# Optimization experiments

Measured on AMD Instinct MI355X. Metric: run time of the kernel, lower is better.

Reference implementation:

```python
import jax, jax.numpy as jnp
import numpy as np
from jax import lax

GAMMA = 1.0
B = 10            # forced by qnn_arch[0]=10 via w1 @ x in feedforward
N_TRAIN = 8192    # kernel support set size


def setup_inputs() -> dict:
    key = jax.random.key(0)
    ks = jax.random.split(key, 20)
    x = jax.random.normal(ks[0], (B, 3, 250, 250), jnp.float32)
    # CNN params (He-ish scale)
    conv1_w = jax.random.normal(ks[1], (6, 3, 5, 5), jnp.float32) * 0.1
    conv1_b = jax.random.normal(ks[2], (6,), jnp.float32) * 0.01
    conv2_w = jax.random.normal(ks[3], (15, 6, 3, 3), jnp.float32) * 0.1
    conv2_b = jax.random.normal(ks[4], (15,), jnp.float32) * 0.01
    fc1_w = jax.random.normal(ks[5], (120, 55815), jnp.float32) * 0.004
    fc1_b = jax.random.normal(ks[6], (120,), jnp.float32) * 0.01
    fc2_w = jax.random.normal(ks[7], (84, 120), jnp.float32) * 0.09
    fc2_b = jax.random.normal(ks[8], (84,), jnp.float32) * 0.01
    fc3_w = jax.random.normal(ks[9], (1, 84), jnp.float32) * 0.1
    fc3_b = jax.random.normal(ks[10], (1,), jnp.float32) * 0.01
    # QNN weights (original uses plain randn)
    qnn_w1 = jax.random.normal(ks[11], (20, 10), jnp.float32)
    qnn_w2 = jax.random.normal(ks[12], (5, 20), jnp.float32)
    # Precomputed training states: tanh(w2 @ tanh(w1 @ f)) per random feature f
    feats = jax.random.normal(ks[13], (N_TRAIN, 10), jnp.float32)
    train_states = jnp.tanh(jnp.tanh(feats @ qnn_w1.T) @ qnn_w2.T)  # [N_TRAIN, 5]
    kcls_w = jax.random.normal(ks[14], (2, N_TRAIN), jnp.float32) * 0.01
    kcls_b = jax.random.normal(ks[15], (2,), jnp.float32) * 0.01
    return {
        'x': x,
        'conv1_w': conv1_w, 'conv1_b': conv1_b,
        'conv2_w': conv2_w, 'conv2_b': conv2_b,
        'fc1_w': fc1_w, 'fc1_b': fc1_b,
        'fc2_w': fc2_w, 'fc2_b': fc2_b,
        'fc3_w': fc3_w, 'fc3_b': fc3_b,
        'qnn_w1': qnn_w1, 'qnn_w2': qnn_w2,
        'train_states': train_states,
        'kcls_w': kcls_w, 'kcls_b': kcls_b,
    }


def _conv(h, w, b, stride, pad):
    out = lax.conv_general_dilated(
        h, w, (stride, stride), [(pad, pad), (pad, pad)],
        dimension_numbers=('NCHW', 'OIHW', 'NCHW'))
    return out + b[None, :, None, None]


def _maxpool_2s1(h):
    return lax.reduce_window(h, -jnp.inf, lax.max, (1, 1, 2, 2), (1, 1, 1, 1), 'VALID')


def reference(x, conv1_w, conv1_b, conv2_w, conv2_b, fc1_w, fc1_b,
              fc2_w, fc2_b, fc3_w, fc3_b, qnn_w1, qnn_w2,
              train_states, kcls_w, kcls_b):
    h = jax.nn.relu(_conv(x, conv1_w, conv1_b, 2, 1))   # [10,6,124,124]
    h = _maxpool_2s1(h)                                 # [10,6,123,123]
    h = jax.nn.relu(_conv(h, conv2_w, conv2_b, 2, 1))   # [10,15,62,62]
    h = _maxpool_2s1(h)                                 # [10,15,61,61]
    h = h.reshape(h.shape[0], -1)                       # [10,55815]
    h = jax.nn.relu(h @ fc1_w.T + fc1_b)                # [10,120]
    h = jax.nn.relu(h @ fc2_w.T + fc2_b)                # [10,84]
    h = h @ fc3_w.T + fc3_b                             # [10,1]
    # QNN feedforward: batch dim B=10 is consumed as the qnn input dim
    s = jnp.tanh(qnn_w1 @ h)                            # [20,1]
    s = jnp.tanh(qnn_w2 @ s)                            # [5,1]
    fs = s[:, 0]                                        # [5]
    # Batched RBF kernel against all train states (replaces the Python .item() loop)
    d2 = jnp.sum((fs[None, :] - train_states) ** 2, axis=-1)  # [N_TRAIN]
    K = jnp.exp(-GAMMA * d2)                            # [N_TRAIN]
    out = K[None, :] @ kcls_w.T + kcls_b                # [1,2]
    return out
```

## Files before the change

### kernel.cpp

```cpp
#include <hip/hip_runtime.h>


#define ACT_STRIDE 55816

__global__ __launch_bounds__(256) void convpool1_k(
    const float* __restrict__ x, const float* __restrict__ w,
    const float* __restrict__ bias, float* __restrict__ out ) {
    const int b   = blockIdx.x;
    const int py0 = blockIdx.y * 4;
    const int px0 = blockIdx.z * 64;
    const int iy0 = 2 * py0 - 1;
    const int ix0 = 2 * px0 - 1;

    __shared__ float sx[3][13][136];

    const int tid = threadIdx.x;

    for (int j = tid; j < 3 * 13 * 133; j += 256) {
        int c  = j % 133;
        int r  = (j / 133) % 13;
        int ic = j / (133 * 13);
        int ix = ix0 + c, iy = iy0 + r;
        float v = 0.f;
        if ((unsigned)ix < 250u && (unsigned)iy < 250u)
            v = x[((size_t)(b * 3 + ic) * 250 + iy) * 250 + ix];
        sx[ic][r][c] = v;
    }
    __syncthreads();

    const int pxl = tid & 63;
    const int pyl = tid >> 6;
    const int py = py0 + pyl, px = px0 + pxl;

    float acc[6][4];
    #pragma unroll
    for (int o = 0; o < 6; ++o) {
        float bv = bias[o];
        #pragma unroll
        for (int q = 0; q < 4; ++q) acc[o][q] = bv;
    }

    #pragma unroll
    for (int ic = 0; ic < 3; ++ic) {
        #pragma unroll
        for (int r = 0; r < 7; ++r) {
            #pragma unroll
            for (int c = 0; c < 7; ++c) {
                float xv = sx[ic][2 * pyl + r][2 * pxl + c];
                #pragma unroll
                for (int dy = 0; dy < 2; ++dy) {
                    int ky = r - 2 * dy;
                    if (ky < 0 || ky >= 5) continue;
                    #pragma unroll
                    for (int dx = 0; dx < 2; ++dx) {
                        int kx = c - 2 * dx;
                        if (kx < 0 || kx >= 5) continue;
                        #pragma unroll
                        for (int o = 0; o < 6; ++o)
                            acc[o][dy * 2 + dx] =
                                fmaf(w[((o * 3 + ic) * 5 + ky) * 5 + kx], xv,
                                     acc[o][dy * 2 + dx]);
                    }
                }
            }
        }
    }

    if (py < 123 && px < 123) {
        #pragma unroll
        for (int o = 0; o < 6; ++o) {
            float m = fmaxf(fmaxf(acc[o][0], acc[o][1]),
                            fmaxf(acc[o][2], acc[o][3]));
            out[((size_t)(b * 6 + o) * 123 + py) * 123 + px] = fmaxf(m, 0.f);
        }
    }
}

__global__ __launch_bounds__(128) void convpool2_k(
    const float* __restrict__ in , const float* __restrict__ w,
    const float* __restrict__ bias, float* __restrict__ out ) {
    const int b   = blockIdx.x;
    const int py0 = blockIdx.y * 2;
    const int px0 = blockIdx.z * 31;
    const int n_py = (61 - py0) < 2 ? (61 - py0) : 2;
    const int n_oy = n_py + 1;
    const int iy0 = 2 * py0 - 1;
    const int ix0 = 2 * px0 - 1;

    __shared__ float sx[6][7][68];
    __shared__ float so[15][3][32];

    const int tid = threadIdx.x;

    for (int j = tid; j < 6 * 7 * 65; j += 128) {
        int col = j % 65;
        int r   = (j / 65) % 7;
        int ic  = j / (65 * 7);
        int ix = ix0 + col, iy = iy0 + r;
        float v = 0.f;
        if ((unsigned)ix < 123u && (unsigned)iy < 123u)
            v = in[((size_t)(b * 6 + ic) * 123 + iy) * 123 + ix];
        sx[ic][r][col] = v;
    }
    __syncthreads();

    for (int p = tid; p < n_oy * 32; p += 128) {
        int oxl = p & 31;
        int oyl = p >> 5;
        if (px0 + oxl < 62) {
            float acc[15];
            #pragma unroll
            for (int o = 0; o < 15; ++o) acc[o] = bias[o];
            #pragma unroll
            for (int ic = 0; ic < 6; ++ic) {
                #pragma unroll
                for (int ky = 0; ky < 3; ++ky) {
                    const float* xr = &sx[ic][2 * oyl + ky][2 * oxl];
                    #pragma unroll
                    for (int kx = 0; kx < 3; ++kx) {
                        float xv = xr[kx];
                        #pragma unroll
                        for (int o = 0; o < 15; ++o)
                            acc[o] += w[((o * 6 + ic) * 3 + ky) * 3 + kx] * xv;
                    }
                }
            }
            #pragma unroll
            for (int o = 0; o < 15; ++o) so[o][oyl][oxl] = fmaxf(acc[o], 0.f);
        }
    }
    __syncthreads();

    for (int j = tid; j < 15 * 2 * 31; j += 128) {
        int pxl = j % 31;
        int pyl = (j / 31) & 1;
        int oc  = j / 62;
        int px = px0 + pxl, py = py0 + pyl;
        if (pyl < n_py && px < 61) {
            float v = fmaxf(fmaxf(so[oc][pyl][pxl],     so[oc][pyl][pxl + 1]),
                            fmaxf(so[oc][pyl + 1][pxl], so[oc][pyl + 1][pxl + 1]));
            out[(size_t)b * ACT_STRIDE + ((size_t)oc * 61 + py) * 61 + px] = v;
        }
    }
}

#define FC1_K      55815
#define FC1_CHUNK  768
#define FC1_NC     73
#define FC1_RT     15

__global__ __launch_bounds__(256) void fc1_partial_k(
    const float* __restrict__ act ,
    const float* __restrict__ w   ,
    float* __restrict__ partials  ) {
    int rt  = blockIdx.x;
    int c   = blockIdx.y;
    int tid = threadIdx.x;
    int wave = tid >> 6, lane = tid & 63;
    int k0 = c * FC1_CHUNK;
    int k1 = k0 + FC1_CHUNK; if (k1 > FC1_K) k1 = FC1_K;
    int r0 = rt * 8 + wave * 2;
    const float* w0 = w + (size_t)r0 * FC1_K;
    const float* w1 = w + (size_t)(r0 + 1) * FC1_K;

    float acc0[10], acc1[10];
    #pragma unroll
    for (int b = 0; b < 10; ++b) { acc0[b] = 0.f; acc1[b] = 0.f; }

    for (int k = k0 + lane * 4; k < k1; k += 256) {
        if (k + 4 <= k1) {
            float4 a4[10];
            #pragma unroll
            for (int b = 0; b < 10; ++b)
                a4[b] = *reinterpret_cast<const float4*>(act + (size_t)b * ACT_STRIDE + k);
            float w00 = w0[k], w01 = w0[k + 1], w02 = w0[k + 2], w03 = w0[k + 3];
            float w10 = w1[k], w11 = w1[k + 1], w12 = w1[k + 2], w13 = w1[k + 3];
            #pragma unroll
            for (int b = 0; b < 10; ++b) {
                acc0[b] += w00 * a4[b].x + w01 * a4[b].y + w02 * a4[b].z + w03 * a4[b].w;
                acc1[b] += w10 * a4[b].x + w11 * a4[b].y + w12 * a4[b].z + w13 * a4[b].w;
            }
        } else {
            for (int j = 0; j < k1 - k; ++j) {
                float wv0 = w0[k + j], wv1 = w1[k + j];
                #pragma unroll
                for (int b = 0; b < 10; ++b) {
                    float av = act[(size_t)b * ACT_STRIDE + k + j];
                    acc0[b] += wv0 * av;
                    acc1[b] += wv1 * av;
                }
            }
        }
    }
    #pragma unroll
    for (int b = 0; b < 10; ++b) {
        float v0 = acc0[b], v1 = acc1[b];
        for (int off = 32; off > 0; off >>= 1) {
            v0 += __shfl_down(v0, off);
            v1 += __shfl_down(v1, off);
        }
        if (lane == 0) {
            size_t base = ((size_t)c * 120 + r0) * 10;
            partials[base + b]      = v0;
            partials[base + 10 + b] = v1;
        }
    }
}

__global__ __launch_bounds__(128) void fcA_k(
    const float* __restrict__ part , const float* __restrict__ fc1_b,
    const float* __restrict__ fc2_w, const float* __restrict__ fc2_b,
    const float* __restrict__ fc3_w, const float* __restrict__ fc3_b,
    float* __restrict__ h3 ) {
    const int b = blockIdx.x;
    const int tid = threadIdx.x;
    __shared__ float s_act[120];
    __shared__ float s_fc2[84];

    if (tid < 120) {
        float s = 0.f;
        for (int c = 0; c < FC1_NC; ++c) s += part[((size_t)c * 120 + tid) * 10 + b];
        s_act[tid] = fmaxf(s + fc1_b[tid], 0.f);
    }
    __syncthreads();
    if (tid < 84) {
        float acc = fc2_b[tid];
        #pragma unroll 4
        for (int k = 0; k < 120; ++k) acc += s_act[k] * fc2_w[tid * 120 + k];
        s_fc2[tid] = fmaxf(acc, 0.f);
    }
    __syncthreads();
    if (tid < 64) {
        float v = s_fc2[tid] * fc3_w[tid];
        if (tid < 20) v += s_fc2[tid + 64] * fc3_w[tid + 64];
        for (int off = 32; off > 0; off >>= 1) v += __shfl_down(v, off);
        if (tid == 0) h3[b] = v + fc3_b[0];
    }
}

__global__ __launch_bounds__(128) void clsB_k(
    const float* __restrict__ h3 ,
    const float* __restrict__ qw1, const float* __restrict__ qw2,
    const float* __restrict__ ts , const float* __restrict__ kw ,
    float* __restrict__ partials ) {
    int tid = threadIdx.x;
    __shared__ float s_h3[10], s_s1[20], s_fs[5];
    if (tid < 10) s_h3[tid] = h3[tid];
    __syncthreads();
    if (tid < 20) {
        float acc = 0.f;
        for (int b = 0; b < 10; ++b) acc += qw1[tid * 10 + b] * s_h3[b];
        s_s1[tid] = tanhf(acc);
    }
    __syncthreads();
    if (tid < 5) {
        float acc = 0.f;
        for (int j = 0; j < 20; ++j) acc += qw2[tid * 20 + j] * s_s1[j];
        s_fs[tid] = tanhf(acc);
    }
    __syncthreads();

    float f0 = s_fs[0], f1 = s_fs[1], f2 = s_fs[2], f3 = s_fs[3], f4 = s_fs[4];
    int n = blockIdx.x * 128 + tid;
    const float* t = ts + (size_t)n * 5;
    float d0 = f0 - t[0], d1 = f1 - t[1], d2 = f2 - t[2], d3 = f3 - t[3], d4 = f4 - t[4];
    float Kv = expf(-(d0 * d0 + d1 * d1 + d2 * d2 + d3 * d3 + d4 * d4));
    float a0 = Kv * kw[n];
    float a1 = Kv * kw[8192 + n];
    for (int off = 32; off > 0; off >>= 1) {
        a0 += __shfl_down(a0, off);
        a1 += __shfl_down(a1, off);
    }
    __shared__ float l0[2], l1[2];
    int wave = tid >> 6, lane = tid & 63;
    if (lane == 0) { l0[wave] = a0; l1[wave] = a1; }
    __syncthreads();
    if (tid == 0) {
        partials[blockIdx.x * 2 + 0] = l0[0] + l0[1];
        partials[blockIdx.x * 2 + 1] = l1[0] + l1[1];
    }
}

__global__ void clsC_k(const float* __restrict__ partials,
                       const float* __restrict__ kb, float* __restrict__ out) {
    int c = threadIdx.x;
    if (c < 2) {
        float acc = kb[c];
        for (int i = 0; i < 64; ++i) acc += partials[i * 2 + c];
        out[c] = acc;
    }
}

extern "C" void kernel_launch(void* const* d_in, const int* in_sizes, int n_in,
                              void* d_out, int out_size, void* d_ws, size_t ws_size,
                              hipStream_t stream) {
    const float* x        = (const float*)d_in[0];
    const float* conv1_w  = (const float*)d_in[1];
    const float* conv1_b  = (const float*)d_in[2];
    const float* conv2_w  = (const float*)d_in[3];
    const float* conv2_b  = (const float*)d_in[4];
    const float* fc1_w    = (const float*)d_in[5];
    const float* fc1_b    = (const float*)d_in[6];
    const float* fc2_w    = (const float*)d_in[7];
    const float* fc2_b    = (const float*)d_in[8];
    const float* fc3_w    = (const float*)d_in[9];
    const float* fc3_b    = (const float*)d_in[10];
    const float* qnn_w1   = (const float*)d_in[11];
    const float* qnn_w2   = (const float*)d_in[12];
    const float* tstates  = (const float*)d_in[13];
    const float* kcls_w   = (const float*)d_in[14];
    const float* kcls_b   = (const float*)d_in[15];

    float* ws = (float*)d_ws;
    float* p1       = ws;
    float* p2       = p1 + 907740;
    float* fc1_part = p2 + 558160;
    float* h3       = fc1_part + 87600;
    float* partials = h3 + 16;

    convpool1_k<<<dim3(10, 31, 2), 256, 0, stream>>>(x, conv1_w, conv1_b, p1);
    convpool2_k<<<dim3(10, 31, 2), 128, 0, stream>>>(p1, conv2_w, conv2_b, p2);
    fc1_partial_k<<<dim3(FC1_RT, FC1_NC), 256, 0, stream>>>(p2, fc1_w, fc1_part);
    fcA_k<<<10, 128, 0, stream>>>(fc1_part, fc1_b, fc2_w, fc2_b, fc3_w, fc3_b, h3);
    clsB_k<<<64, 128, 0, stream>>>(h3, qnn_w1, qnn_w2, tstates, kcls_w, partials);
    clsC_k<<<1, 64, 0, stream>>>(partials, kcls_b, (float*)d_out);
}
```

Measured before the change: 91.52 us.

## Restructure conv1 so each thread computes a conv-output column and pools via shuffles

```diff
diff --git a/kernel.cpp b/kernel.cpp
--- a/kernel.cpp
+++ b/kernel.cpp
@@ -7,19 +7,19 @@
     const float* __restrict__ x, const float* __restrict__ w,
     const float* __restrict__ bias, float* __restrict__ out ) {
     const int b   = blockIdx.x;
-    const int py0 = blockIdx.y * 4;
-    const int px0 = blockIdx.z * 64;
+    const int py0 = blockIdx.y * 8;
+    const int px0 = blockIdx.z * 63;
     const int iy0 = 2 * py0 - 1;
     const int ix0 = 2 * px0 - 1;
 
-    __shared__ float sx[3][13][136];
+    __shared__ float sx[3][21][132];
 
     const int tid = threadIdx.x;
 
-    for (int j = tid; j < 3 * 13 * 133; j += 256) {
-        int c  = j % 133;
-        int r  = (j / 133) % 13;
-        int ic = j / (133 * 13);
+    for (int j = tid; j < 3 * 21 * 131; j += 256) {
+        int c  = j % 131;
+        int r  = (j / 131) % 21;
+        int ic = j / (131 * 21);
         int ix = ix0 + c, iy = iy0 + r;
         float v = 0.f;
         if ((unsigned)ix < 250u && (unsigned)iy < 250u)
@@ -28,50 +28,50 @@
     }
     __syncthreads();
 
-    const int pxl = tid & 63;
-    const int pyl = tid >> 6;
-    const int py = py0 + pyl, px = px0 + pxl;
-
-    float acc[6][4];
-    #pragma unroll
-    for (int o = 0; o < 6; ++o) {
-        float bv = bias[o];
+    const int lane = tid & 63;
+    const int wv   = tid >> 6;
+
+    float acc[3][6];
+    #pragma unroll
+    for (int j = 0; j < 3; ++j)
         #pragma unroll
-        for (int q = 0; q < 4; ++q) acc[o][q] = bv;
-    }
+        for (int o = 0; o < 6; ++o) acc[j][o] = bias[o];
 
     #pragma unroll
     for (int ic = 0; ic < 3; ++ic) {
         #pragma unroll
-        for (int r = 0; r < 7; ++r) {
-            #pragma unroll
-            for (int c = 0; c < 7; ++c) {
-                float xv = sx[ic][2 * pyl + r][2 * pxl + c];
-                #pragma unroll
-                for (int dy = 0; dy < 2; ++dy) {
-                    int ky = r - 2 * dy;
-                    if (ky < 0 || ky >= 5) continue;
+        for (int r = 0; r < 9; ++r) {
+            float xr[5];
+            #pragma unroll
+            for (int c = 0; c < 5; ++c)
+                xr[c] = sx[ic][4 * wv + r][2 * lane + c];
+            #pragma unroll
+            for (int j = 0; j < 3; ++j) {
+                int ky = r - 2 * j;
+                if (ky >= 0 && ky < 5) {
                     #pragma unroll
-                    for (int dx = 0; dx < 2; ++dx) {
-                        int kx = c - 2 * dx;
-                        if (kx < 0 || kx >= 5) continue;
+                    for (int c = 0; c < 5; ++c) {
                         #pragma unroll
                         for (int o = 0; o < 6; ++o)
-                            acc[o][dy * 2 + dx] =
-                                fmaf(w[((o * 3 + ic) * 5 + ky) * 5 + kx], xv,
-                                     acc[o][dy * 2 + dx]);
+                            acc[j][o] = fmaf(w[((o * 3 + ic) * 5 + ky) * 5 + c],
+                                             xr[c], acc[j][o]);
                     }
                 }
             }
         }
     }
 
-    if (py < 123 && px < 123) {
+    #pragma unroll
+    for (int j = 0; j < 2; ++j) {
+        const int py = py0 + 2 * wv + j;
+        const int px = px0 + lane;
         #pragma unroll
         for (int o = 0; o < 6; ++o) {
-            float m = fmaxf(fmaxf(acc[o][0], acc[o][1]),
-                            fmaxf(acc[o][2], acc[o][3]));
-            out[((size_t)(b * 6 + o) * 123 + py) * 123 + px] = fmaxf(m, 0.f);
+            float m  = fmaxf(acc[j][o], acc[j + 1][o]);
+            float nb = __shfl_down(m, 1);
+            if (lane < 63 && py < 123 && px < 123)
+                out[((size_t)(b * 6 + o) * 123 + py) * 123 + px] =
+                    fmaxf(fmaxf(m, nb), 0.f);
         }
     }
 }
@@ -318,7 +318,7 @@
     float* h3       = fc1_part + 87600;
     float* partials = h3 + 16;
 
-    convpool1_k<<<dim3(10, 31, 2), 256, 0, stream>>>(x, conv1_w, conv1_b, p1);
+    convpool1_k<<<dim3(10, 16, 2), 256, 0, stream>>>(x, conv1_w, conv1_b, p1);
     convpool2_k<<<dim3(10, 31, 2), 128, 0, stream>>>(p1, conv2_w, conv2_b, p2);
     fc1_partial_k<<<dim3(FC1_RT, FC1_NC), 256, 0, stream>>>(p2, fc1_w, fc1_part);
     fcA_k<<<10, 128, 0, stream>>>(fc1_part, fc1_b, fc2_w, fc2_b, fc3_w, fc3_b, h3);
```

New measurement: 85.76 us. 1.07x faster.
